# Kernel optimization log

Measured on AMD Instinct MI355X. Metric: run time of the kernel, lower is better.

## Reference

```python
import jax, jax.numpy as jnp
import numpy as np

H = 12          # trees_num / n_heads
D_WEIGHT = 0.1  # opt['d_weight']
NEG = -1e9


def setup_inputs() -> dict:
    key = jax.random.key(0)
    ks = jax.random.split(key, 6)
    B, N, D = 8, 512, 768
    inp = {}
    inp["input"] = jax.random.normal(ks[0], (B, N, D), dtype=jnp.float32)
    inp["src_mask"] = jax.random.randint(ks[1], (B, 1, N), 0, 2).astype(jnp.int32)
    inp["dep_emb"] = jax.random.normal(ks[2], (B, N, N), dtype=jnp.float32)
    s = 1.0 / np.sqrt(D)
    inp["Wq"] = jax.random.normal(ks[3], (D, D), dtype=jnp.float32) * s
    inp["bq"] = jnp.zeros((D,), dtype=jnp.float32)
    inp["Wk"] = jax.random.normal(ks[4], (D, D), dtype=jnp.float32) * s
    inp["bk"] = jnp.zeros((D,), dtype=jnp.float32)
    return inp


def reference(input, src_mask, dep_emb, Wq, bq, Wk, bk):
    B, N, D = input.shape
    dk = D // H
    # Q/K projections -> [B, H, N, dk]
    q = (input @ Wq + bq).reshape(B, N, H, dk).transpose(0, 2, 1, 3)
    k = (input @ Wk + bk).reshape(B, N, H, dk).transpose(0, 2, 1, 3)
    # scaled scores [B, H, N, N]
    scores = jnp.einsum("bhqd,bhkd->bhqk", q, k) / jnp.sqrt(jnp.asarray(dk, input.dtype))
    # blend with dependency bias: dep_emb [B,N,N] -> [B,1,N,N]
    scores = (1.0 - D_WEIGHT) * scores + D_WEIGHT * dep_emb[:, None, :, :]
    # mask: src_mask [B,1,N] -> [B,1,1,N]; masked_fill(mask==0, -1e9)
    scores = jnp.where(src_mask[:, None, :, :] == 0, NEG, scores)
    p_attn = jax.nn.softmax(scores, axis=-1)  # [B, H, N, N]
    # original returns list of per-head [B,N,N]; full tensor is equivalent
    return p_attn
```

## Files before the change

### kernel.cpp

```cpp
#include <hip/hip_runtime.h>


typedef _Float16 f16;
typedef _Float16 f16x4 __attribute__((ext_vector_type(4)));
typedef _Float16 f16x8 __attribute__((ext_vector_type(8)));
typedef float    f32x4 __attribute__((ext_vector_type(4)));

#define NTOK   512
#define DMODEL 768
#define BATCH  8
#define NHEAD  12
#define NEGV   (-1e9f)
#define KPAD   72

__global__ __launch_bounds__(256)
void prep_kernel(const float* __restrict__ X, f16* __restrict__ Xh,
                 const float* __restrict__ Wq, const float* __restrict__ Wk,
                 f16* __restrict__ Wt) {
    const int bx = blockIdx.x;
    if (bx < 3072) {
        const size_t i = ((size_t)bx * 256 + threadIdx.x) * 4;
        float4 v = *(const float4*)&X[i];
        f16x4 h = { (f16)v.x, (f16)v.y, (f16)v.z, (f16)v.w };
        *(f16x4*)&Xh[i] = h;
    } else {
        __shared__ float tile[32][33];
        const int id = bx - 3072;
        const int kb = (id % 24) * 32;
        const int nb = (id / 24) * 32;
        const float* __restrict__ W = (nb < 768) ? Wq : Wk;
        const int nc = (nb < 768) ? nb : nb - 768;
        const int tx = threadIdx.x & 31, ty = threadIdx.x >> 5;
        #pragma unroll
        for (int i = 0; i < 4; ++i)
            tile[ty + i*8][tx] = W[(size_t)(kb + ty + i*8) * DMODEL + nc + tx];
        __syncthreads();
        #pragma unroll
        for (int i = 0; i < 4; ++i)
            Wt[(size_t)(nb + ty + i*8) * DMODEL + kb + tx] = (f16)tile[tx][ty + i*8];
    }
}

__global__ __launch_bounds__(64)
void proj_mfma(const f16* __restrict__ Xh, const f16* __restrict__ Wt,
               const float* __restrict__ bq, const float* __restrict__ bk,
               f16* __restrict__ QK) {
    const int m0 = blockIdx.x * 64;
    const int n0 = blockIdx.y * 64;
    const int l = threadIdx.x;
    const int l15 = l & 15, quad = l >> 4;

    f32x4 acc[4][4];
    #pragma unroll
    for (int i = 0; i < 4; ++i)
        #pragma unroll
        for (int j = 0; j < 4; ++j) acc[i][j] = (f32x4){0.f, 0.f, 0.f, 0.f};

    const f16* __restrict__ Ab = Xh + (size_t)(m0 + l15) * DMODEL + quad * 8;
    const f16* __restrict__ Bb = Wt + (size_t)(n0 + l15) * DMODEL + quad * 8;

    for (int ks = 0; ks < DMODEL / 32; ++ks) {
        f16x8 a[4], b[4];
        #pragma unroll
        for (int mi = 0; mi < 4; ++mi)
            a[mi] = *(const f16x8*)(Ab + (size_t)mi * 16 * DMODEL + ks * 32);
        #pragma unroll
        for (int ni = 0; ni < 4; ++ni)
            b[ni] = *(const f16x8*)(Bb + (size_t)ni * 16 * DMODEL + ks * 32);
        #pragma unroll
        for (int mi = 0; mi < 4; ++mi)
            #pragma unroll
            for (int ni = 0; ni < 4; ++ni)
                acc[mi][ni] = __builtin_amdgcn_mfma_f32_16x16x32_f16(
                    a[mi], b[ni], acc[mi][ni], 0, 0, 0);
    }

    const float* __restrict__ bias = (n0 < 768) ? (bq + n0) : (bk + n0 - 768);
    #pragma unroll
    for (int ni = 0; ni < 4; ++ni) {
        const float bv = bias[ni * 16 + l15];
        const int col = n0 + ni * 16 + l15;
        #pragma unroll
        for (int mi = 0; mi < 4; ++mi)
            #pragma unroll
            for (int r = 0; r < 4; ++r) {
                const int row = m0 + mi * 16 + quad * 4 + r;
                QK[(size_t)row * 1536 + col] = (f16)(acc[mi][ni][r] + bv);
            }
    }
}

__global__ __launch_bounds__(256, 2)
void attn_mfma(const f16* __restrict__ QK, const float* __restrict__ dep,
               const int* __restrict__ mask, float* __restrict__ out) {
    const int qt = blockIdx.x, h = blockIdx.y, b = blockIdx.z;
    const int tid = threadIdx.x;
    const int wid = tid >> 6;
    const int l = tid & 63;
    const int l15 = l & 15, quad = l >> 4;
    const int q0 = qt * 64 + wid * 16;

    __shared__ f16 Ks[NTOK * KPAD];

    {
        const f16* __restrict__ Ksrc = QK + (size_t)b * NTOK * 1536 + 768 + h * 64;
        #pragma unroll
        for (int c = 0; c < 16; ++c) {
            const int chunk = tid + c * 256;
            const int token = chunk >> 3;
            const int part  = chunk & 7;
            f16x8 v = *(const f16x8*)(Ksrc + (size_t)token * 1536 + part * 8);
            *(f16x8*)&Ks[token * KPAD + part * 8] = v;
        }
    }
    __syncthreads();

    f32x4 acc[32];
    #pragma unroll
    for (int t = 0; t < 32; ++t) acc[t] = (f32x4){0.f, 0.f, 0.f, 0.f};

    const f16* __restrict__ Qb = QK + (size_t)(b * NTOK + q0 + l15) * 1536 + h * 64 + quad * 8;

    #pragma unroll
    for (int ks = 0; ks < 2; ++ks) {
        f16x8 a = *(const f16x8*)(Qb + ks * 32);
        #pragma unroll
        for (int t = 0; t < 32; ++t) {
            f16x8 bf = *(const f16x8*)&Ks[(t * 16 + l15) * KPAD + ks * 32 + quad * 8];
            acc[t] = __builtin_amdgcn_mfma_f32_16x16x32_f16(a, bf, acc[t], 0, 0, 0);
        }
    }

    const float SC = (1.0f - 0.1f) / 8.0f;
    const float DW = 0.1f;
    const float* __restrict__ deprow = dep + ((size_t)b * NTOK + q0 + quad * 4) * NTOK;
    const int*   __restrict__ mrow   = mask + b * NTOK;
    #pragma unroll
    for (int t = 0; t < 32; ++t) {
        const int col = t * 16 + l15;
        const int mv = mrow[col];
        #pragma unroll
        for (int r = 0; r < 4; ++r) {
            const float dv = deprow[(size_t)r * NTOK + col];
            const float s = SC * acc[t][r] + DW * dv;
            acc[t][r] = mv ? s : NEGV;
        }
    }

    float rmax[4] = {NEGV, NEGV, NEGV, NEGV};
    #pragma unroll
    for (int t = 0; t < 32; ++t)
        #pragma unroll
        for (int r = 0; r < 4; ++r) rmax[r] = fmaxf(rmax[r], acc[t][r]);
    #pragma unroll
    for (int r = 0; r < 4; ++r) {
        rmax[r] = fmaxf(rmax[r], __shfl_xor(rmax[r], 1));
        rmax[r] = fmaxf(rmax[r], __shfl_xor(rmax[r], 2));
        rmax[r] = fmaxf(rmax[r], __shfl_xor(rmax[r], 4));
        rmax[r] = fmaxf(rmax[r], __shfl_xor(rmax[r], 8));
    }
    float rsum[4] = {0.f, 0.f, 0.f, 0.f};
    #pragma unroll
    for (int t = 0; t < 32; ++t)
        #pragma unroll
        for (int r = 0; r < 4; ++r) {
            const float e = __expf(acc[t][r] - rmax[r]);
            acc[t][r] = e;
            rsum[r] += e;
        }
    #pragma unroll
    for (int r = 0; r < 4; ++r) {
        rsum[r] += __shfl_xor(rsum[r], 1);
        rsum[r] += __shfl_xor(rsum[r], 2);
        rsum[r] += __shfl_xor(rsum[r], 4);
        rsum[r] += __shfl_xor(rsum[r], 8);
    }
    float inv[4];
    #pragma unroll
    for (int r = 0; r < 4; ++r) inv[r] = 1.0f / rsum[r];

    float* __restrict__ orow = out + ((size_t)((b * NHEAD + h) * NTOK) + q0 + quad * 4) * NTOK;
    #pragma unroll
    for (int t = 0; t < 32; ++t)
        #pragma unroll
        for (int r = 0; r < 4; ++r)
            orow[(size_t)r * NTOK + t * 16 + l15] = acc[t][r] * inv[r];
}

extern "C" void kernel_launch(void* const* d_in, const int* in_sizes, int n_in,
                              void* d_out, int out_size, void* d_ws, size_t ws_size,
                              hipStream_t stream) {
    const float* X    = (const float*)d_in[0];
    const int*   mask = (const int*)  d_in[1];
    const float* dep  = (const float*)d_in[2];
    const float* Wq   = (const float*)d_in[3];
    const float* bq   = (const float*)d_in[4];
    const float* Wk   = (const float*)d_in[5];
    const float* bk   = (const float*)d_in[6];
    float* out = (float*)d_out;

    f16* Xh = (f16*)d_ws;
    f16* Wt = Xh + (size_t)BATCH * NTOK * DMODEL;
    f16* QK = Wt + (size_t)1536 * DMODEL;

    prep_kernel<<<dim3(3072 + 1152), 256, 0, stream>>>(X, Xh, Wq, Wk, Wt);
    proj_mfma<<<dim3((BATCH * NTOK) / 64, 1536 / 64), 64, 0, stream>>>(Xh, Wt, bq, bk, QK);
    attn_mfma<<<dim3(NTOK / 64, NHEAD, BATCH), 256, 0, stream>>>(QK, dep, mask, out);
}
```

Measured before the change: 191.5 us.

## Tile projection GEMM through LDS and transpose attention MFMA for vectorized row I/O

The projection kernel moves from 64-thread blocks that load operands straight from global memory to 256-thread blocks computing 128x128 tiles staged in shared memory, so operand loads are shared across four waves. The attention kernel swaps the MFMA operand order so each lane holds four consecutive key columns of one query row. This lets dep and mask be read and the output written as float4/int4, and reduces the softmax reductions to two cross-quad shuffles. The goal is cutting strided scalar global traffic, which dominates this memory-bound output, at the cost of more shared memory and barriers in the GEMM.

```diff
diff --git a/kernel.cpp b/kernel.cpp
--- a/kernel.cpp
+++ b/kernel.cpp
@@ -41,14 +41,20 @@
     }
 }
 
-__global__ __launch_bounds__(64)
+__global__ __launch_bounds__(256)
 void proj_mfma(const f16* __restrict__ Xh, const f16* __restrict__ Wt,
                const float* __restrict__ bq, const float* __restrict__ bk,
                f16* __restrict__ QK) {
-    const int m0 = blockIdx.x * 64;
-    const int n0 = blockIdx.y * 64;
-    const int l = threadIdx.x;
+    const int m0 = blockIdx.x * 128;
+    const int n0 = blockIdx.y * 128;
+    const int tid = threadIdx.x;
+    const int wid = tid >> 6, l = tid & 63;
     const int l15 = l & 15, quad = l >> 4;
+    const int wm = (wid & 1) * 64;
+    const int wn = (wid >> 1) * 64;
+
+    __shared__ f16 As[128 * KPAD];
+    __shared__ f16 Bs[128 * KPAD];
 
     f32x4 acc[4][4];
     #pragma unroll
@@ -56,35 +62,51 @@
         #pragma unroll
         for (int j = 0; j < 4; ++j) acc[i][j] = (f32x4){0.f, 0.f, 0.f, 0.f};
 
-    const f16* __restrict__ Ab = Xh + (size_t)(m0 + l15) * DMODEL + quad * 8;
-    const f16* __restrict__ Bb = Wt + (size_t)(n0 + l15) * DMODEL + quad * 8;
-
-    for (int ks = 0; ks < DMODEL / 32; ++ks) {
-        f16x8 a[4], b[4];
+    const int srow  = tid >> 1;
+    const int scol  = (tid & 1) * 32;
+
+    for (int kt = 0; kt < DMODEL; kt += 64) {
+        const f16* __restrict__ Asrc = Xh + (size_t)(m0 + srow) * DMODEL + kt + scol;
+        const f16* __restrict__ Bsrc = Wt + (size_t)(n0 + srow) * DMODEL + kt + scol;
+        #pragma unroll
+        for (int j = 0; j < 4; ++j) {
+            f16x8 av = *(const f16x8*)(Asrc + j * 8);
+            *(f16x8*)&As[srow * KPAD + scol + j * 8] = av;
+        }
+        #pragma unroll
+        for (int j = 0; j < 4; ++j) {
+            f16x8 bv = *(const f16x8*)(Bsrc + j * 8);
+            *(f16x8*)&Bs[srow * KPAD + scol + j * 8] = bv;
+        }
+        __syncthreads();
+        #pragma unroll
+        for (int ks = 0; ks < 2; ++ks) {
+            f16x8 a[4], b[4];
+            #pragma unroll
+            for (int mi = 0; mi < 4; ++mi)
+                a[mi] = *(f16x8*)&As[(wm + mi*16 + l15) * KPAD + ks*32 + quad*8];
+            #pragma unroll
+            for (int ni = 0; ni < 4; ++ni)
+                b[ni] = *(f16x8*)&Bs[(wn + ni*16 + l15) * KPAD + ks*32 + quad*8];
+            #pragma unroll
+            for (int mi = 0; mi < 4; ++mi)
+                #pragma unroll
+                for (int ni = 0; ni < 4; ++ni)
+                    acc[mi][ni] = __builtin_amdgcn_mfma_f32_16x16x32_f16(
+                        a[mi], b[ni], acc[mi][ni], 0, 0, 0);
+        }
+        __syncthreads();
+    }
+
+    #pragma unroll
+    for (int ni = 0; ni < 4; ++ni) {
+        const int col = n0 + wn + ni * 16 + l15;
+        const float bv = (col < 768) ? bq[col] : bk[col - 768];
         #pragma unroll
         for (int mi = 0; mi < 4; ++mi)
-            a[mi] = *(const f16x8*)(Ab + (size_t)mi * 16 * DMODEL + ks * 32);
-        #pragma unroll
-        for (int ni = 0; ni < 4; ++ni)
-            b[ni] = *(const f16x8*)(Bb + (size_t)ni * 16 * DMODEL + ks * 32);
-        #pragma unroll
-        for (int mi = 0; mi < 4; ++mi)
-            #pragma unroll
-            for (int ni = 0; ni < 4; ++ni)
-                acc[mi][ni] = __builtin_amdgcn_mfma_f32_16x16x32_f16(
-                    a[mi], b[ni], acc[mi][ni], 0, 0, 0);
-    }
-
-    const float* __restrict__ bias = (n0 < 768) ? (bq + n0) : (bk + n0 - 768);
-    #pragma unroll
-    for (int ni = 0; ni < 4; ++ni) {
-        const float bv = bias[ni * 16 + l15];
-        const int col = n0 + ni * 16 + l15;
-        #pragma unroll
-        for (int mi = 0; mi < 4; ++mi)
             #pragma unroll
             for (int r = 0; r < 4; ++r) {
-                const int row = m0 + mi * 16 + quad * 4 + r;
+                const int row = m0 + wm + mi * 16 + quad * 4 + r;
                 QK[(size_t)row * 1536 + col] = (f16)(acc[mi][ni][r] + bv);
             }
     }
@@ -95,10 +117,9 @@
                const int* __restrict__ mask, float* __restrict__ out) {
     const int qt = blockIdx.x, h = blockIdx.y, b = blockIdx.z;
     const int tid = threadIdx.x;
-    const int wid = tid >> 6;
-    const int l = tid & 63;
+    const int wid = tid >> 6, l = tid & 63;
     const int l15 = l & 15, quad = l >> 4;
-    const int q0 = qt * 64 + wid * 16;
+    const int qrow = qt * 64 + wid * 16 + l15;
 
     __shared__ f16 Ks[NTOK * KPAD];
 
@@ -119,72 +140,60 @@
     #pragma unroll
     for (int t = 0; t < 32; ++t) acc[t] = (f32x4){0.f, 0.f, 0.f, 0.f};
 
-    const f16* __restrict__ Qb = QK + (size_t)(b * NTOK + q0 + l15) * 1536 + h * 64 + quad * 8;
-
-    #pragma unroll
-    for (int ks = 0; ks < 2; ++ks) {
-        f16x8 a = *(const f16x8*)(Qb + ks * 32);
-        #pragma unroll
-        for (int t = 0; t < 32; ++t) {
-            f16x8 bf = *(const f16x8*)&Ks[(t * 16 + l15) * KPAD + ks * 32 + quad * 8];
-            acc[t] = __builtin_amdgcn_mfma_f32_16x16x32_f16(a, bf, acc[t], 0, 0, 0);
-        }
+    const f16* __restrict__ Qb = QK + (size_t)(b * NTOK + qrow) * 1536 + h * 64 + quad * 8;
+    const f16x8 qf0 = *(const f16x8*)(Qb);
+    const f16x8 qf1 = *(const f16x8*)(Qb + 32);
+
+    #pragma unroll
+    for (int t = 0; t < 32; ++t) {
+        f16x8 k0 = *(f16x8*)&Ks[(t * 16 + l15) * KPAD + quad * 8];
+        acc[t] = __builtin_amdgcn_mfma_f32_16x16x32_f16(k0, qf0, acc[t], 0, 0, 0);
+        f16x8 k1 = *(f16x8*)&Ks[(t * 16 + l15) * KPAD + 32 + quad * 8];
+        acc[t] = __builtin_amdgcn_mfma_f32_16x16x32_f16(k1, qf1, acc[t], 0, 0, 0);
     }
 
     const float SC = (1.0f - 0.1f) / 8.0f;
     const float DW = 0.1f;
-    const float* __restrict__ deprow = dep + ((size_t)b * NTOK + q0 + quad * 4) * NTOK;
+    const float* __restrict__ deprow = dep + ((size_t)b * NTOK + qrow) * NTOK;
     const int*   __restrict__ mrow   = mask + b * NTOK;
     #pragma unroll
     for (int t = 0; t < 32; ++t) {
-        const int col = t * 16 + l15;
-        const int mv = mrow[col];
+        const int c0 = t * 16 + quad * 4;
+        const int4   mv = *(const int4*)  &mrow[c0];
+        const float4 dv = *(const float4*)&deprow[c0];
+        acc[t][0] = mv.x ? SC * acc[t][0] + DW * dv.x : NEGV;
+        acc[t][1] = mv.y ? SC * acc[t][1] + DW * dv.y : NEGV;
+        acc[t][2] = mv.z ? SC * acc[t][2] + DW * dv.z : NEGV;
+        acc[t][3] = mv.w ? SC * acc[t][3] + DW * dv.w : NEGV;
+    }
+
+    float m = NEGV;
+    #pragma unroll
+    for (int t = 0; t < 32; ++t)
+        #pragma unroll
+        for (int r = 0; r < 4; ++r) m = fmaxf(m, acc[t][r]);
+    m = fmaxf(m, __shfl_xor(m, 16));
+    m = fmaxf(m, __shfl_xor(m, 32));
+
+    float s = 0.f;
+    #pragma unroll
+    for (int t = 0; t < 32; ++t)
         #pragma unroll
         for (int r = 0; r < 4; ++r) {
-            const float dv = deprow[(size_t)r * NTOK + col];
-            const float s = SC * acc[t][r] + DW * dv;
-            acc[t][r] = mv ? s : NEGV;
-        }
-    }
-
-    float rmax[4] = {NEGV, NEGV, NEGV, NEGV};
-    #pragma unroll
-    for (int t = 0; t < 32; ++t)
-        #pragma unroll
-        for (int r = 0; r < 4; ++r) rmax[r] = fmaxf(rmax[r], acc[t][r]);
-    #pragma unroll
-    for (int r = 0; r < 4; ++r) {
-        rmax[r] = fmaxf(rmax[r], __shfl_xor(rmax[r], 1));
-        rmax[r] = fmaxf(rmax[r], __shfl_xor(rmax[r], 2));
-        rmax[r] = fmaxf(rmax[r], __shfl_xor(rmax[r], 4));
-        rmax[r] = fmaxf(rmax[r], __shfl_xor(rmax[r], 8));
-    }
-    float rsum[4] = {0.f, 0.f, 0.f, 0.f};
-    #pragma unroll
-    for (int t = 0; t < 32; ++t)
-        #pragma unroll
-        for (int r = 0; r < 4; ++r) {
-            const float e = __expf(acc[t][r] - rmax[r]);
+            const float e = __expf(acc[t][r] - m);
             acc[t][r] = e;
-            rsum[r] += e;
-        }
-    #pragma unroll
-    for (int r = 0; r < 4; ++r) {
-        rsum[r] += __shfl_xor(rsum[r], 1);
-        rsum[r] += __shfl_xor(rsum[r], 2);
-        rsum[r] += __shfl_xor(rsum[r], 4);
-        rsum[r] += __shfl_xor(rsum[r], 8);
-    }
-    float inv[4];
-    #pragma unroll
-    for (int r = 0; r < 4; ++r) inv[r] = 1.0f / rsum[r];
-
-    float* __restrict__ orow = out + ((size_t)((b * NHEAD + h) * NTOK) + q0 + quad * 4) * NTOK;
-    #pragma unroll
-    for (int t = 0; t < 32; ++t)
-        #pragma unroll
-        for (int r = 0; r < 4; ++r)
-            orow[(size_t)r * NTOK + t * 16 + l15] = acc[t][r] * inv[r];
+            s += e;
+        }
+    s += __shfl_xor(s, 16);
+    s += __shfl_xor(s, 32);
+    const float inv = 1.0f / s;
+
+    float* __restrict__ orow = out + ((size_t)((b * NHEAD + h) * NTOK) + qrow) * NTOK;
+    #pragma unroll
+    for (int t = 0; t < 32; ++t) {
+        float4 p = { acc[t][0] * inv, acc[t][1] * inv, acc[t][2] * inv, acc[t][3] * inv };
+        *(float4*)&orow[t * 16 + quad * 4] = p;
+    }
 }
 
 extern "C" void kernel_launch(void* const* d_in, const int* in_sizes, int n_in,
@@ -204,6 +213,6 @@
     f16* QK = Wt + (size_t)1536 * DMODEL;
 
     prep_kernel<<<dim3(3072 + 1152), 256, 0, stream>>>(X, Xh, Wq, Wk, Wt);
-    proj_mfma<<<dim3((BATCH * NTOK) / 64, 1536 / 64), 64, 0, stream>>>(Xh, Wt, bq, bk, QK);
+    proj_mfma<<<dim3(4096 / 128, 1536 / 128), 256, 0, stream>>>(Xh, Wt, bq, bk, QK);
     attn_mfma<<<dim3(NTOK / 64, NHEAD, BATCH), 256, 0, stream>>>(QK, dep, mask, out);
 }
```

New measurement: 235.5 us. +23.0%, slower.

## Tile projection GEMM through LDS and enlarge attention blocks to 128 queries

Applied to the files above, without the earlier changes.

The projection GEMM now uses 128x128 tiles with four waves that stage A and B sub-tiles in shared memory, so each global load is reused across waves instead of every wave streaming its own rows from global memory. The score scale is folded into Q at projection time, which removes a multiply in the attention epilogue. The attention kernel moves to 512-thread blocks covering 128 queries, so each staged K tile serves twice as many query rows. The cost is extra LDS traffic and barrier syncs in the GEMM, fewer GEMM blocks, and higher register and LDS pressure per attention block.

```diff
diff --git a/kernel.cpp b/kernel.cpp
--- a/kernel.cpp
+++ b/kernel.cpp
@@ -41,14 +41,20 @@
     }
 }
 
-__global__ __launch_bounds__(64)
+__global__ __launch_bounds__(256)
 void proj_mfma(const f16* __restrict__ Xh, const f16* __restrict__ Wt,
                const float* __restrict__ bq, const float* __restrict__ bk,
                f16* __restrict__ QK) {
-    const int m0 = blockIdx.x * 64;
-    const int n0 = blockIdx.y * 64;
-    const int l = threadIdx.x;
+    const int m0 = blockIdx.x * 128;
+    const int n0 = blockIdx.y * 128;
+    const int tid = threadIdx.x;
+    const int wid = tid >> 6, l = tid & 63;
     const int l15 = l & 15, quad = l >> 4;
+    const int wm = (wid & 1) * 64;
+    const int wn = (wid >> 1) * 64;
+
+    __shared__ f16 As[128 * KPAD];
+    __shared__ f16 Bs[128 * KPAD];
 
     f32x4 acc[4][4];
     #pragma unroll
@@ -56,57 +62,75 @@
         #pragma unroll
         for (int j = 0; j < 4; ++j) acc[i][j] = (f32x4){0.f, 0.f, 0.f, 0.f};
 
-    const f16* __restrict__ Ab = Xh + (size_t)(m0 + l15) * DMODEL + quad * 8;
-    const f16* __restrict__ Bb = Wt + (size_t)(n0 + l15) * DMODEL + quad * 8;
-
-    for (int ks = 0; ks < DMODEL / 32; ++ks) {
-        f16x8 a[4], b[4];
+    const int srow = tid >> 1;
+    const int scol = (tid & 1) * 32;
+
+    for (int kt = 0; kt < DMODEL; kt += 64) {
+        const f16* __restrict__ Asrc = Xh + (size_t)(m0 + srow) * DMODEL + kt + scol;
+        const f16* __restrict__ Bsrc = Wt + (size_t)(n0 + srow) * DMODEL + kt + scol;
+        #pragma unroll
+        for (int j = 0; j < 4; ++j) {
+            f16x8 av = *(const f16x8*)(Asrc + j * 8);
+            *(f16x8*)&As[srow * KPAD + scol + j * 8] = av;
+        }
+        #pragma unroll
+        for (int j = 0; j < 4; ++j) {
+            f16x8 bv = *(const f16x8*)(Bsrc + j * 8);
+            *(f16x8*)&Bs[srow * KPAD + scol + j * 8] = bv;
+        }
+        __syncthreads();
+        #pragma unroll
+        for (int ks = 0; ks < 2; ++ks) {
+            f16x8 a[4], b[4];
+            #pragma unroll
+            for (int mi = 0; mi < 4; ++mi)
+                a[mi] = *(f16x8*)&As[(wm + mi*16 + l15) * KPAD + ks*32 + quad*8];
+            #pragma unroll
+            for (int ni = 0; ni < 4; ++ni)
+                b[ni] = *(f16x8*)&Bs[(wn + ni*16 + l15) * KPAD + ks*32 + quad*8];
+            #pragma unroll
+            for (int mi = 0; mi < 4; ++mi)
+                #pragma unroll
+                for (int ni = 0; ni < 4; ++ni)
+                    acc[mi][ni] = __builtin_amdgcn_mfma_f32_16x16x32_f16(
+                        a[mi], b[ni], acc[mi][ni], 0, 0, 0);
+        }
+        __syncthreads();
+    }
+
+    const float SC = (1.0f - 0.1f) / 8.0f;
+    #pragma unroll
+    for (int ni = 0; ni < 4; ++ni) {
+        const int col = n0 + wn + ni * 16 + l15;
+        const bool isQ = (col < 768);
+        const float bv = isQ ? bq[col] : bk[col - 768];
+        const float sc = isQ ? SC : 1.0f;
         #pragma unroll
         for (int mi = 0; mi < 4; ++mi)
-            a[mi] = *(const f16x8*)(Ab + (size_t)mi * 16 * DMODEL + ks * 32);
-        #pragma unroll
-        for (int ni = 0; ni < 4; ++ni)
-            b[ni] = *(const f16x8*)(Bb + (size_t)ni * 16 * DMODEL + ks * 32);
-        #pragma unroll
-        for (int mi = 0; mi < 4; ++mi)
-            #pragma unroll
-            for (int ni = 0; ni < 4; ++ni)
-                acc[mi][ni] = __builtin_amdgcn_mfma_f32_16x16x32_f16(
-                    a[mi], b[ni], acc[mi][ni], 0, 0, 0);
-    }
-
-    const float* __restrict__ bias = (n0 < 768) ? (bq + n0) : (bk + n0 - 768);
-    #pragma unroll
-    for (int ni = 0; ni < 4; ++ni) {
-        const float bv = bias[ni * 16 + l15];
-        const int col = n0 + ni * 16 + l15;
-        #pragma unroll
-        for (int mi = 0; mi < 4; ++mi)
             #pragma unroll
             for (int r = 0; r < 4; ++r) {
-                const int row = m0 + mi * 16 + quad * 4 + r;
-                QK[(size_t)row * 1536 + col] = (f16)(acc[mi][ni][r] + bv);
+                const int row = m0 + wm + mi * 16 + quad * 4 + r;
+                QK[(size_t)row * 1536 + col] = (f16)((acc[mi][ni][r] + bv) * sc);
             }
     }
 }
 
-__global__ __launch_bounds__(256, 2)
+__global__ __launch_bounds__(512, 4)
 void attn_mfma(const f16* __restrict__ QK, const float* __restrict__ dep,
                const int* __restrict__ mask, float* __restrict__ out) {
     const int qt = blockIdx.x, h = blockIdx.y, b = blockIdx.z;
     const int tid = threadIdx.x;
-    const int wid = tid >> 6;
-    const int l = tid & 63;
+    const int wid = tid >> 6, l = tid & 63;
     const int l15 = l & 15, quad = l >> 4;
-    const int q0 = qt * 64 + wid * 16;
+    const int q0 = qt * 128 + wid * 16;
 
     __shared__ f16 Ks[NTOK * KPAD];
 
     {
         const f16* __restrict__ Ksrc = QK + (size_t)b * NTOK * 1536 + 768 + h * 64;
         #pragma unroll
-        for (int c = 0; c < 16; ++c) {
-            const int chunk = tid + c * 256;
+        for (int c = 0; c < 8; ++c) {
+            const int chunk = tid + c * 512;
             const int token = chunk >> 3;
             const int part  = chunk & 7;
             f16x8 v = *(const f16x8*)(Ksrc + (size_t)token * 1536 + part * 8);
@@ -120,18 +144,17 @@
     for (int t = 0; t < 32; ++t) acc[t] = (f32x4){0.f, 0.f, 0.f, 0.f};
 
     const f16* __restrict__ Qb = QK + (size_t)(b * NTOK + q0 + l15) * 1536 + h * 64 + quad * 8;
-
-    #pragma unroll
-    for (int ks = 0; ks < 2; ++ks) {
-        f16x8 a = *(const f16x8*)(Qb + ks * 32);
-        #pragma unroll
-        for (int t = 0; t < 32; ++t) {
-            f16x8 bf = *(const f16x8*)&Ks[(t * 16 + l15) * KPAD + ks * 32 + quad * 8];
-            acc[t] = __builtin_amdgcn_mfma_f32_16x16x32_f16(a, bf, acc[t], 0, 0, 0);
-        }
-    }
-
-    const float SC = (1.0f - 0.1f) / 8.0f;
+    const f16x8 qf0 = *(const f16x8*)(Qb);
+    const f16x8 qf1 = *(const f16x8*)(Qb + 32);
+
+    #pragma unroll
+    for (int t = 0; t < 32; ++t) {
+        f16x8 k0 = *(f16x8*)&Ks[(t * 16 + l15) * KPAD + quad * 8];
+        acc[t] = __builtin_amdgcn_mfma_f32_16x16x32_f16(qf0, k0, acc[t], 0, 0, 0);
+        f16x8 k1 = *(f16x8*)&Ks[(t * 16 + l15) * KPAD + 32 + quad * 8];
+        acc[t] = __builtin_amdgcn_mfma_f32_16x16x32_f16(qf1, k1, acc[t], 0, 0, 0);
+    }
+
     const float DW = 0.1f;
     const float* __restrict__ deprow = dep + ((size_t)b * NTOK + q0 + quad * 4) * NTOK;
     const int*   __restrict__ mrow   = mask + b * NTOK;
@@ -142,7 +165,7 @@
         #pragma unroll
         for (int r = 0; r < 4; ++r) {
             const float dv = deprow[(size_t)r * NTOK + col];
-            const float s = SC * acc[t][r] + DW * dv;
+            const float s = acc[t][r] + DW * dv;
             acc[t][r] = mv ? s : NEGV;
         }
     }
@@ -204,6 +227,6 @@
     f16* QK = Wt + (size_t)1536 * DMODEL;
 
     prep_kernel<<<dim3(3072 + 1152), 256, 0, stream>>>(X, Xh, Wq, Wk, Wt);
-    proj_mfma<<<dim3((BATCH * NTOK) / 64, 1536 / 64), 64, 0, stream>>>(Xh, Wt, bq, bk, QK);
-    attn_mfma<<<dim3(NTOK / 64, NHEAD, BATCH), 256, 0, stream>>>(QK, dep, mask, out);
-}
+    proj_mfma<<<dim3(4096 / 128, 1536 / 128), 256, 0, stream>>>(Xh, Wt, bq, bk, QK);
+    attn_mfma<<<dim3(NTOK / 128, NHEAD, BATCH), 512, 0, stream>>>(QK, dep, mask, out);
+}
```

New measurement: 240.7 us. +25.7%, slower.
